# Kernel optimization log

Hardware: AMD Instinct MI355X
Metric: run time of the kernel (lower is better)

Reference implementation:

```python
import jax, jax.numpy as jnp
import numpy as np

N_SAMPLES = 8192
EMBED_DIM = 128
NUM_CLASSES = 100


def setup_inputs() -> dict:
    key = jax.random.key(0)
    k1, k2 = jax.random.split(key)
    x = jax.random.normal(k1, (N_SAMPLES, EMBED_DIM), dtype=jnp.float32)
    # FastAP assumes L2-normalized embeddings (dist2 = 2 - 2*cos in [0, 4])
    x = x / jnp.linalg.norm(x, axis=1, keepdims=True)
    labels = jax.random.randint(k2, (N_SAMPLES,), 0, NUM_CLASSES, dtype=jnp.int64 if jax.config.jax_enable_x64 else jnp.int32)
    return {"batch": x, "labels": labels, "num_bins": 10}


def reference(batch, labels, num_bins):
    N = batch.shape[0]
    L = num_bins + 1                      # number of histogram bin centers (edges of linspace)
    Delta = 4.0 / num_bins                # bin width
    Z = jnp.linspace(0.0, 4.0, L)

    same = labels[:, None] == labels[None, :]
    eye = jnp.eye(N, dtype=bool)
    I_pos = (same & ~eye).astype(batch.dtype)   # Aff > 0
    I_neg = (~same).astype(batch.dtype)         # Aff < 0 (diag is 'same', so excluded)
    N_pos = I_pos.sum(axis=1)

    # squared euclidean distance for unit-norm rows: 2 - 2*cos
    dist2 = 2.0 - 2.0 * (batch @ batch.T)       # [N, N]

    # soft-binning histogram: one N x N pulse per bin, reduced to per-row counts.
    # lax.map keeps only one [N, N] pulse buffer alive at a time.
    def bin_fn(z):
        pulse = jnp.maximum(0.0, 1.0 - jnp.abs(dist2 - z) / Delta)
        return (jnp.einsum('ij,ij->i', pulse, I_pos),
                jnp.einsum('ij,ij->i', pulse, I_neg))

    hp, hn = jax.lax.map(bin_fn, Z)             # each [L, N]
    h_pos = hp.T                                # [N, L]
    h_neg = hn.T

    H_pos = jnp.cumsum(h_pos, axis=1)
    H = jnp.cumsum(h_pos + h_neg, axis=1)

    # FastAP = h_pos * H_pos / H, with NaN/Inf (H == 0) zeroed, as in the original
    safe_H = jnp.where(H > 0, H, 1.0)
    ap = jnp.where(H > 0, h_pos * H_pos / safe_H, 0.0).sum(axis=1)

    # divide by N_pos; rows with no positives are dropped from the mean
    valid = N_pos > 0
    safe_Np = jnp.where(valid, N_pos, 1.0)
    ap = jnp.where(valid, ap / safe_Np, 0.0)

    n_valid = valid.sum().astype(batch.dtype)
    loss = 1.0 - ap.sum() / n_valid
    return loss
```

## Files before the change

### kernel.cpp

```cpp
#include <hip/hip_runtime.h>

#define NS 8192
#define EMBED 128
#define ROWCHUNK 512
#define NPANEL (ROWCHUNK / 32)
#define AROW 12
#define INV64K (1.0f / 65536.0f)

typedef __bf16 bf16x8 __attribute__((ext_vector_type(8)));
typedef float f32x4 __attribute__((ext_vector_type(4)));
typedef float f32x2 __attribute__((ext_vector_type(2)));
typedef const __attribute__((address_space(1))) unsigned ag_u32;
typedef __attribute__((address_space(3))) unsigned al_u32;

#define OFF_XB    0u
#define OFF_GS    2097152u
#define OFF_GSP   2228224u
#define OFF_GA    2359296u
#define OFF_GAP   2752512u
#define OFF_AC    3145728u
#define OFF_CNT   3145792u
#define OFF_OFS   3146304u
#define OFF_INTRA 3146816u
#define OFF_CLS   3179584u
#define ZERO_U4   65537u

__device__ inline float clamp01(float x) { return __builtin_amdgcn_fmed3f(x, 0.f, 1.f); }
__device__ inline f32x2 pkclamp01(f32x2 v) {
  return __builtin_elementwise_min(__builtin_elementwise_max(v, (f32x2){0.f, 0.f}),
                                   (f32x2){1.f, 1.f});
}
__device__ inline unsigned short f2bf(float f) {
  unsigned u = __float_as_uint(f);
  u += 0x7fffu + ((u >> 16) & 1u);
  return (unsigned short)(u >> 16);
}

__global__ __launch_bounds__(256) void prep_count_kernel(const int* __restrict__ labels,
                                                         int* __restrict__ cnt,
                                                         int* __restrict__ ofs,
                                                         int* __restrict__ intra) {
  __shared__ int c[128];
  const int tid = threadIdx.x;
  if (tid < 128) c[tid] = 0;
  __syncthreads();
  for (int i = tid; i < NS; i += 256)
    intra[i] = atomicAdd(&c[labels[i]], 1);
  __syncthreads();
  if (tid == 0) {
    int run = 0;
    for (int k = 0; k < 128; ++k) { ofs[k] = run; cnt[k] = c[k]; run += c[k]; }
  }
}

__global__ __launch_bounds__(256) void prep_scatter_kernel(
    const float* __restrict__ x, const int* __restrict__ labels,
    const int* __restrict__ ofs, const int* __restrict__ intra,
    unsigned short* __restrict__ xb, int* __restrict__ classOf,
    uint4* __restrict__ zbase) {
  const int gid = blockIdx.x * 256 + threadIdx.x;
  const int row = gid >> 4, g = gid & 15;
  const int lab = labels[row];
  const int slot = ofs[lab] + intra[row];
  const float4 v0 = reinterpret_cast<const float4*>(x)[row * 32 + g * 2];
  const float4 v1 = reinterpret_cast<const float4*>(x)[row * 32 + g * 2 + 1];
  uint4 o;
  o.x = (unsigned)f2bf(v0.x) | ((unsigned)f2bf(v0.y) << 16);
  o.y = (unsigned)f2bf(v0.z) | ((unsigned)f2bf(v0.w) << 16);
  o.z = (unsigned)f2bf(v1.x) | ((unsigned)f2bf(v1.y) << 16);
  o.w = (unsigned)f2bf(v1.z) | ((unsigned)f2bf(v1.w) << 16);
  reinterpret_cast<uint4*>(xb)[slot * 16 + (g ^ (slot & 7))] = o;
  if (g == 0) classOf[slot] = lab;
  if (gid < (int)ZERO_U4) zbase[gid] = make_uint4(0u, 0u, 0u, 0u);
}

__global__ __launch_bounds__(256, 8) void fastap_main_kernel(
    const unsigned short* __restrict__ xb,
    const int* __restrict__ classOf, const int* __restrict__ cnt,
    const int* __restrict__ ofs,
    unsigned* __restrict__ gS, unsigned* __restrict__ gSp,
    unsigned* __restrict__ gA, unsigned* __restrict__ gAp) {
  __shared__ __align__(16) unsigned short sA[2][32 * 128];

  const int tid  = threadIdx.x;
  const int wave = tid >> 6;
  const int lane = tid & 63;
  const int l16  = lane & 15;
  const int quad = lane >> 4;
  const int colBase  = blockIdx.x * 64;
  const int rowChunk = blockIdx.y * ROWCHUNK;

  const int jcol = colBase + wave * 16 + l16;
  bf16x8 bfr[4];
  #pragma unroll
  for (int kb = 0; kb < 4; ++kb) {
    const int pg = (kb * 4 + quad) ^ (l16 & 7);
    bfr[kb] = *reinterpret_cast<const bf16x8*>(&xb[jcol * 128 + pg * 8]);
  }
  const int ci = classOf[jcol];
  const int lo = ofs[ci];
  const int hi = lo + cnt[ci];

  f32x2 C01 = {0.f, 0.f}, C23 = {0.f, 0.f};
  f32x2 Cp01 = {0.f, 0.f}, Cp23 = {0.f, 0.f};

  int aOff[4];
  #pragma unroll
  for (int kb = 0; kb < 4; ++kb)
    aOff[kb] = l16 * 128 + (((kb * 4 + quad) ^ (l16 & 7)) << 3);

  const unsigned short* xrb = xb + rowChunk * 128;
  auto stage = [&](int p, int b) {
    const unsigned short* src = xrb + p * (32 * 128);
    __builtin_amdgcn_global_load_lds((ag_u32*)(src + tid * 8),
                                     (al_u32*)(&sA[b][tid * 8]), 16, 0, 0);
    __builtin_amdgcn_global_load_lds((ag_u32*)(src + (tid + 256) * 8),
                                     (al_u32*)(&sA[b][(tid + 256) * 8]), 16, 0, 0);
  };

  auto tile16 = [&](const unsigned short* ap, int lcr) {
    bf16x8 a0 = *reinterpret_cast<const bf16x8*>(&ap[aOff[0]]);
    bf16x8 a1 = *reinterpret_cast<const bf16x8*>(&ap[aOff[1]]);
    bf16x8 a2 = *reinterpret_cast<const bf16x8*>(&ap[aOff[2]]);
    bf16x8 a3 = *reinterpret_cast<const bf16x8*>(&ap[aOff[3]]);
    f32x4 acc = {0.f, 0.f, 0.f, 0.f};
    acc = __builtin_amdgcn_mfma_f32_16x16x32_bf16(a0, bfr[0], acc, 0, 0, 0);
    acc = __builtin_amdgcn_mfma_f32_16x16x32_bf16(a1, bfr[1], acc, 0, 0, 0);
    acc = __builtin_amdgcn_mfma_f32_16x16x32_bf16(a2, bfr[2], acc, 0, 0, 0);
    acc = __builtin_amdgcn_mfma_f32_16x16x32_bf16(a3, bfr[3], acc, 0, 0, 0);

    const int i0 = rowChunk + lcr + quad * 4;

    if (__builtin_expect((hi > i0) & (lo < i0 + 4), 0)) {
      #pragma unroll
      for (int r = 0; r < 4; ++r) {
        const float a = acc[r];
        const int i = i0 + r;
        const float pm = (i >= lo && i < hi) ? 1.f : 0.f;
        const f32x2 av = {a, a}, p2 = {pm, pm};
        const f32x2 d01 = pkclamp01(__builtin_elementwise_fma(av, (f32x2){5.f, 5.f},
                                                              (f32x2){-1.f, 0.f}));
        const f32x2 d23 = pkclamp01(__builtin_elementwise_fma(av, (f32x2){5.f, 5.f},
                                                              (f32x2){1.f, 2.f}));
        C01 += d01; C23 += d23;
        Cp01 = __builtin_elementwise_fma(p2, d01, Cp01);
        Cp23 = __builtin_elementwise_fma(p2, d23, Cp23);
      }
    } else {
      #pragma unroll
      for (int r = 0; r < 4; ++r) {
        const f32x2 av = {acc[r], acc[r]};
        C01 += pkclamp01(__builtin_elementwise_fma(av, (f32x2){5.f, 5.f},
                                                   (f32x2){-1.f, 0.f}));
        C23 += pkclamp01(__builtin_elementwise_fma(av, (f32x2){5.f, 5.f},
                                                   (f32x2){1.f, 2.f}));
      }
    }

    const float mabs = fmaxf(fmaxf(fabsf(acc[0]), fabsf(acc[1])),
                             fmaxf(fabsf(acc[2]), fabsf(acc[3])));
    if (__builtin_expect(mabs > 0.4f, 0)) {
      #pragma unroll
      for (int r = 0; r < 4; ++r) {
        const float a = acc[r];
        if (fabsf(a) <= 0.4f) continue;
        const int i = i0 + r;
        const float d0 = clamp01(fmaf(a, 5.f, -1.f));
        const float d1 = clamp01(a * 5.f);
        const float d2 = clamp01(fmaf(a, 5.f, 1.f));
        const float d3 = clamp01(fmaf(a, 5.f, 2.f));
        if (i == jcol) {
          C01 -= (f32x2){d0, d1};  C23 -= (f32x2){d2, d3};
          Cp01 -= (f32x2){d0, d1}; Cp23 -= (f32x2){d2, d3};
          #pragma unroll
          for (int k = 7; k <= 10; ++k)
            atomicAdd(&gA[jcol * AROW + k], (unsigned)(-65536));
        } else {
          const bool isPos = (i >= lo) & (i < hi);
          const float t = fmaf(a, -5.f, 5.f);
          #pragma unroll
          for (int k = 0; k <= 2; ++k) {
            const int q = (int)(clamp01((float)(k + 1) - t) * 65536.f + 0.5f);
            if (q) {
              atomicAdd(&gA[jcol * AROW + k], (unsigned)q);
              if (isPos) atomicAdd(&gAp[jcol * AROW + k], (unsigned)q);
            }
          }
          #pragma unroll
          for (int k = 7; k <= 10; ++k) {
            const int q = (int)((clamp01((float)(k + 1) - t) - 1.f) * 65536.f - 0.5f);
            if (q) {
              atomicAdd(&gA[jcol * AROW + k], (unsigned)q);
              if (isPos) atomicAdd(&gAp[jcol * AROW + k], (unsigned)q);
            }
          }
        }
      }
    }
  };

  stage(0, 0);
  __syncthreads();

  #pragma unroll 1
  for (int p = 0; p < NPANEL; ++p) {
    const int cur = p & 1;
    if (p + 1 < NPANEL) stage(p + 1, cur ^ 1);
    tile16(&sA[cur][0],        p * 32);
    tile16(&sA[cur][16 * 128], p * 32 + 16);
    __syncthreads();
  }

  #pragma unroll
  for (int m = 16; m < 64; m <<= 1) {
    C01.x  += __shfl_xor(C01.x,  m, 64); C01.y  += __shfl_xor(C01.y,  m, 64);
    C23.x  += __shfl_xor(C23.x,  m, 64); C23.y  += __shfl_xor(C23.y,  m, 64);
    Cp01.x += __shfl_xor(Cp01.x, m, 64); Cp01.y += __shfl_xor(Cp01.y, m, 64);
    Cp23.x += __shfl_xor(Cp23.x, m, 64); Cp23.y += __shfl_xor(Cp23.y, m, 64);
  }

  if (quad == 0) {
    const float Cv[4]  = {C01.x, C01.y, C23.x, C23.y};
    const float Cpv[4] = {Cp01.x, Cp01.y, Cp23.x, Cp23.y};
    #pragma unroll
    for (int k = 0; k < 4; ++k) {
      atomicAdd(&gS[jcol * 4 + k],  (unsigned)(int)lrintf(Cv[k]  * 65536.f));
      atomicAdd(&gSp[jcol * 4 + k], (unsigned)(int)lrintf(Cpv[k] * 65536.f));
    }
  }
}

__global__ __launch_bounds__(256) void epilogue_kernel(
    const unsigned* __restrict__ gS, const unsigned* __restrict__ gSp,
    const unsigned* __restrict__ gA, const unsigned* __restrict__ gAp,
    const int* __restrict__ classOf, const int* __restrict__ cnt,
    float* __restrict__ accum, unsigned* __restrict__ done,
    float* __restrict__ out) {
  const int i = blockIdx.x * 256 + threadIdx.x;
  const int np = cnt[classOf[i]] - 1;
  float ap = 0.f, val = 0.f, HpPrev = 0.f;
  #pragma unroll
  for (int b = 0; b <= 10; ++b) {
    const float baseH  = (b < 3) ? 0.f
                       : (b < 7) ? (float)(int)gS[i * 4 + (b - 3)]  * INV64K : 8192.f;
    const float basePp = (b < 3) ? 0.f
                       : (b < 7) ? (float)(int)gSp[i * 4 + (b - 3)] * INV64K : (float)np;
    const float H  = baseH  + (float)(int)gA[i * AROW + b]  * INV64K;
    const float Hp = basePp + (float)(int)gAp[i * AROW + b] * INV64K;
    const float hp = Hp - HpPrev;
    HpPrev = Hp;
    if (H > 1e-6f) ap += hp * Hp / H;
  }
  if (np > 0) { ap /= (float)np; val = 1.f; } else ap = 0.f;

  __shared__ float sa[256], sv[256];
  sa[threadIdx.x] = ap; sv[threadIdx.x] = val;
  __syncthreads();
  for (int s = 128; s > 0; s >>= 1) {
    if (threadIdx.x < s) {
      sa[threadIdx.x] += sa[threadIdx.x + s];
      sv[threadIdx.x] += sv[threadIdx.x + s];
    }
    __syncthreads();
  }
  if (threadIdx.x == 0) {
    atomicAdd(&accum[0], sa[0]);
    atomicAdd(&accum[1], sv[0]);
    __threadfence();
    const unsigned prev = atomicAdd(done, 1u);
    if (prev == gridDim.x - 1) {
      const float a = atomicAdd(&accum[0], 0.f);
      const float c = atomicAdd(&accum[1], 0.f);
      out[0] = 1.f - (c > 0.f ? a / c : 0.f);
    }
  }
}

extern "C" void kernel_launch(void* const* d_in, const int* in_sizes, int n_in,
                              void* d_out, int out_size, void* d_ws, size_t ws_size,
                              hipStream_t stream) {
  const float* x      = (const float*)d_in[0];
  const int*   labels = (const int*)d_in[1];
  float* out = (float*)d_out;

  char* ws = (char*)d_ws;
  unsigned short* xb = (unsigned short*)(ws + OFF_XB);
  unsigned* gS    = (unsigned*)(ws + OFF_GS);
  unsigned* gSp   = (unsigned*)(ws + OFF_GSP);
  unsigned* gA    = (unsigned*)(ws + OFF_GA);
  unsigned* gAp   = (unsigned*)(ws + OFF_GAP);
  float*    accum = (float*)(ws + OFF_AC);
  unsigned* done  = (unsigned*)(ws + OFF_AC + 8);
  int*      cnt   = (int*)(ws + OFF_CNT);
  int*      ofs   = (int*)(ws + OFF_OFS);
  int*      intra = (int*)(ws + OFF_INTRA);
  int*      cls   = (int*)(ws + OFF_CLS);

  prep_count_kernel<<<1, 256, 0, stream>>>(labels, cnt, ofs, intra);
  prep_scatter_kernel<<<512, 256, 0, stream>>>(x, labels, ofs, intra, xb, cls,
                                               (uint4*)(ws + OFF_GS));
  fastap_main_kernel<<<dim3(NS / 64, NS / ROWCHUNK), 256, 0, stream>>>(
      xb, cls, cnt, ofs, gS, gSp, gA, gAp);
  epilogue_kernel<<<NS / 256, 256, 0, stream>>>(gS, gSp, gA, gAp, cls, cnt,
                                                accum, done, out);
}
```

Before: 118.2 us.

## Compute two column tiles per wave and parallelize label counting across blocks

The main kernel now has each wave handle 32 columns (two 16-column B fragments) instead of 16. Each A fragment loaded from LDS feeds eight MFMAs instead of four, and the row chunk is halved to 256 so the grid keeps a similar block count. Launch bounds are relaxed to 6 blocks per SM to make room for the doubled accumulator registers. The single-block label count is replaced by a multi-block kernel that uses global atomics, a memset and a last-block-done prefix sum. This removes a serial launch, but adds a memset and the atomic contention that comes with it.

```diff
diff --git a/kernel.cpp b/kernel.cpp
--- a/kernel.cpp
+++ b/kernel.cpp
@@ -2,7 +2,7 @@
 
 #define NS 8192
 #define EMBED 128
-#define ROWCHUNK 512
+#define ROWCHUNK 256
 #define NPANEL (ROWCHUNK / 32)
 #define AROW 12
 #define INV64K (1.0f / 65536.0f)
@@ -21,8 +21,9 @@
 #define OFF_AC    3145728u
 #define OFF_CNT   3145792u
 #define OFF_OFS   3146304u
-#define OFF_INTRA 3146816u
-#define OFF_CLS   3179584u
+#define OFF_PD    3146816u
+#define OFF_INTRA 3146880u
+#define OFF_CLS   3179648u
 #define ZERO_U4   65537u
 
 __device__ inline float clamp01(float x) { return __builtin_amdgcn_fmed3f(x, 0.f, 1.f); }
@@ -39,17 +40,23 @@
 __global__ __launch_bounds__(256) void prep_count_kernel(const int* __restrict__ labels,
                                                          int* __restrict__ cnt,
                                                          int* __restrict__ ofs,
-                                                         int* __restrict__ intra) {
+                                                         int* __restrict__ intra,
+                                                         unsigned* __restrict__ pdone) {
+  const int gid = blockIdx.x * 256 + threadIdx.x;
+  intra[gid] = atomicAdd(&cnt[labels[gid]], 1);
+  __threadfence();
   __shared__ int c[128];
-  const int tid = threadIdx.x;
-  if (tid < 128) c[tid] = 0;
+  __shared__ unsigned last;
   __syncthreads();
-  for (int i = tid; i < NS; i += 256)
-    intra[i] = atomicAdd(&c[labels[i]], 1);
+  if (threadIdx.x == 0) last = (atomicAdd(pdone, 1u) == gridDim.x - 1) ? 1u : 0u;
   __syncthreads();
-  if (tid == 0) {
-    int run = 0;
-    for (int k = 0; k < 128; ++k) { ofs[k] = run; cnt[k] = c[k]; run += c[k]; }
+  if (last) {
+    if (threadIdx.x < 128) c[threadIdx.x] = atomicAdd(&cnt[threadIdx.x], 0);
+    __syncthreads();
+    if (threadIdx.x == 0) {
+      int run = 0;
+      for (int k = 0; k < 128; ++k) { ofs[k] = run; run += c[k]; }
+    }
   }
 }
 
@@ -74,7 +81,7 @@
   if (gid < (int)ZERO_U4) zbase[gid] = make_uint4(0u, 0u, 0u, 0u);
 }
 
-__global__ __launch_bounds__(256, 8) void fastap_main_kernel(
+__global__ __launch_bounds__(256, 6) void fastap_main_kernel(
     const unsigned short* __restrict__ xb,
     const int* __restrict__ classOf, const int* __restrict__ cnt,
     const int* __restrict__ ofs,
@@ -87,22 +94,23 @@
   const int lane = tid & 63;
   const int l16  = lane & 15;
   const int quad = lane >> 4;
-  const int colBase  = blockIdx.x * 64;
+  const int colBase  = blockIdx.x * 128;
   const int rowChunk = blockIdx.y * ROWCHUNK;
 
-  const int jcol = colBase + wave * 16 + l16;
-  bf16x8 bfr[4];
+  const int jc1 = colBase + wave * 32 + l16;
+  const int jc2 = jc1 + 16;
+  bf16x8 bf1[4], bf2[4];
   #pragma unroll
   for (int kb = 0; kb < 4; ++kb) {
     const int pg = (kb * 4 + quad) ^ (l16 & 7);
-    bfr[kb] = *reinterpret_cast<const bf16x8*>(&xb[jcol * 128 + pg * 8]);
-  }
-  const int ci = classOf[jcol];
-  const int lo = ofs[ci];
-  const int hi = lo + cnt[ci];
-
-  f32x2 C01 = {0.f, 0.f}, C23 = {0.f, 0.f};
-  f32x2 Cp01 = {0.f, 0.f}, Cp23 = {0.f, 0.f};
+    bf1[kb] = *reinterpret_cast<const bf16x8*>(&xb[jc1 * 128 + pg * 8]);
+    bf2[kb] = *reinterpret_cast<const bf16x8*>(&xb[jc2 * 128 + pg * 8]);
+  }
+  const int ci1 = classOf[jc1], lo1 = ofs[ci1], hi1 = lo1 + cnt[ci1];
+  const int ci2 = classOf[jc2], lo2 = ofs[ci2], hi2 = lo2 + cnt[ci2];
+
+  f32x2 C01a = {0.f,0.f}, C23a = {0.f,0.f}, Cp01a = {0.f,0.f}, Cp23a = {0.f,0.f};
+  f32x2 C01b = {0.f,0.f}, C23b = {0.f,0.f}, Cp01b = {0.f,0.f}, Cp23b = {0.f,0.f};
 
   int aOff[4];
   #pragma unroll
@@ -118,19 +126,8 @@
                                      (al_u32*)(&sA[b][(tid + 256) * 8]), 16, 0, 0);
   };
 
-  auto tile16 = [&](const unsigned short* ap, int lcr) {
-    bf16x8 a0 = *reinterpret_cast<const bf16x8*>(&ap[aOff[0]]);
-    bf16x8 a1 = *reinterpret_cast<const bf16x8*>(&ap[aOff[1]]);
-    bf16x8 a2 = *reinterpret_cast<const bf16x8*>(&ap[aOff[2]]);
-    bf16x8 a3 = *reinterpret_cast<const bf16x8*>(&ap[aOff[3]]);
-    f32x4 acc = {0.f, 0.f, 0.f, 0.f};
-    acc = __builtin_amdgcn_mfma_f32_16x16x32_bf16(a0, bfr[0], acc, 0, 0, 0);
-    acc = __builtin_amdgcn_mfma_f32_16x16x32_bf16(a1, bfr[1], acc, 0, 0, 0);
-    acc = __builtin_amdgcn_mfma_f32_16x16x32_bf16(a2, bfr[2], acc, 0, 0, 0);
-    acc = __builtin_amdgcn_mfma_f32_16x16x32_bf16(a3, bfr[3], acc, 0, 0, 0);
-
-    const int i0 = rowChunk + lcr + quad * 4;
-
+  auto group = [&](const f32x4& acc, int jc, int lo, int hi, int i0,
+                   f32x2& C01, f32x2& C23, f32x2& Cp01, f32x2& Cp23) {
     if (__builtin_expect((hi > i0) & (lo < i0 + 4), 0)) {
       #pragma unroll
       for (int r = 0; r < 4; ++r) {
@@ -169,12 +166,12 @@
         const float d1 = clamp01(a * 5.f);
         const float d2 = clamp01(fmaf(a, 5.f, 1.f));
         const float d3 = clamp01(fmaf(a, 5.f, 2.f));
-        if (i == jcol) {
+        if (i == jc) {
           C01 -= (f32x2){d0, d1};  C23 -= (f32x2){d2, d3};
           Cp01 -= (f32x2){d0, d1}; Cp23 -= (f32x2){d2, d3};
           #pragma unroll
           for (int k = 7; k <= 10; ++k)
-            atomicAdd(&gA[jcol * AROW + k], (unsigned)(-65536));
+            atomicAdd(&gA[jc * AROW + k], (unsigned)(-65536));
         } else {
           const bool isPos = (i >= lo) & (i < hi);
           const float t = fmaf(a, -5.f, 5.f);
@@ -182,21 +179,41 @@
           for (int k = 0; k <= 2; ++k) {
             const int q = (int)(clamp01((float)(k + 1) - t) * 65536.f + 0.5f);
             if (q) {
-              atomicAdd(&gA[jcol * AROW + k], (unsigned)q);
-              if (isPos) atomicAdd(&gAp[jcol * AROW + k], (unsigned)q);
+              atomicAdd(&gA[jc * AROW + k], (unsigned)q);
+              if (isPos) atomicAdd(&gAp[jc * AROW + k], (unsigned)q);
             }
           }
           #pragma unroll
           for (int k = 7; k <= 10; ++k) {
             const int q = (int)((clamp01((float)(k + 1) - t) - 1.f) * 65536.f - 0.5f);
             if (q) {
-              atomicAdd(&gA[jcol * AROW + k], (unsigned)q);
-              if (isPos) atomicAdd(&gAp[jcol * AROW + k], (unsigned)q);
+              atomicAdd(&gA[jc * AROW + k], (unsigned)q);
+              if (isPos) atomicAdd(&gAp[jc * AROW + k], (unsigned)q);
             }
           }
         }
       }
     }
+  };
+
+  auto tile16 = [&](const unsigned short* ap, int lcr) {
+    bf16x8 a0 = *reinterpret_cast<const bf16x8*>(&ap[aOff[0]]);
+    bf16x8 a1 = *reinterpret_cast<const bf16x8*>(&ap[aOff[1]]);
+    bf16x8 a2 = *reinterpret_cast<const bf16x8*>(&ap[aOff[2]]);
+    bf16x8 a3 = *reinterpret_cast<const bf16x8*>(&ap[aOff[3]]);
+    f32x4 acc1 = {0.f, 0.f, 0.f, 0.f}, acc2 = {0.f, 0.f, 0.f, 0.f};
+    acc1 = __builtin_amdgcn_mfma_f32_16x16x32_bf16(a0, bf1[0], acc1, 0, 0, 0);
+    acc1 = __builtin_amdgcn_mfma_f32_16x16x32_bf16(a1, bf1[1], acc1, 0, 0, 0);
+    acc1 = __builtin_amdgcn_mfma_f32_16x16x32_bf16(a2, bf1[2], acc1, 0, 0, 0);
+    acc1 = __builtin_amdgcn_mfma_f32_16x16x32_bf16(a3, bf1[3], acc1, 0, 0, 0);
+    acc2 = __builtin_amdgcn_mfma_f32_16x16x32_bf16(a0, bf2[0], acc2, 0, 0, 0);
+    acc2 = __builtin_amdgcn_mfma_f32_16x16x32_bf16(a1, bf2[1], acc2, 0, 0, 0);
+    acc2 = __builtin_amdgcn_mfma_f32_16x16x32_bf16(a2, bf2[2], acc2, 0, 0, 0);
+    acc2 = __builtin_amdgcn_mfma_f32_16x16x32_bf16(a3, bf2[3], acc2, 0, 0, 0);
+
+    const int i0 = rowChunk + lcr + quad * 4;
+    group(acc1, jc1, lo1, hi1, i0, C01a, C23a, Cp01a, Cp23a);
+    group(acc2, jc2, lo2, hi2, i0, C01b, C23b, Cp01b, Cp23b);
   };
 
   stage(0, 0);
@@ -213,19 +230,27 @@
 
   #pragma unroll
   for (int m = 16; m < 64; m <<= 1) {
-    C01.x  += __shfl_xor(C01.x,  m, 64); C01.y  += __shfl_xor(C01.y,  m, 64);
-    C23.x  += __shfl_xor(C23.x,  m, 64); C23.y  += __shfl_xor(C23.y,  m, 64);
-    Cp01.x += __shfl_xor(Cp01.x, m, 64); Cp01.y += __shfl_xor(Cp01.y, m, 64);
-    Cp23.x += __shfl_xor(Cp23.x, m, 64); Cp23.y += __shfl_xor(Cp23.y, m, 64);
+    C01a.x += __shfl_xor(C01a.x, m, 64); C01a.y += __shfl_xor(C01a.y, m, 64);
+    C23a.x += __shfl_xor(C23a.x, m, 64); C23a.y += __shfl_xor(C23a.y, m, 64);
+    Cp01a.x += __shfl_xor(Cp01a.x, m, 64); Cp01a.y += __shfl_xor(Cp01a.y, m, 64);
+    Cp23a.x += __shfl_xor(Cp23a.x, m, 64); Cp23a.y += __shfl_xor(Cp23a.y, m, 64);
+    C01b.x += __shfl_xor(C01b.x, m, 64); C01b.y += __shfl_xor(C01b.y, m, 64);
+    C23b.x += __shfl_xor(C23b.x, m, 64); C23b.y += __shfl_xor(C23b.y, m, 64);
+    Cp01b.x += __shfl_xor(Cp01b.x, m, 64); Cp01b.y += __shfl_xor(Cp01b.y, m, 64);
+    Cp23b.x += __shfl_xor(Cp23b.x, m, 64); Cp23b.y += __shfl_xor(Cp23b.y, m, 64);
   }
 
   if (quad == 0) {
-    const float Cv[4]  = {C01.x, C01.y, C23.x, C23.y};
-    const float Cpv[4] = {Cp01.x, Cp01.y, Cp23.x, Cp23.y};
+    const float Cv1[4]  = {C01a.x, C01a.y, C23a.x, C23a.y};
+    const float Cpv1[4] = {Cp01a.x, Cp01a.y, Cp23a.x, Cp23a.y};
+    const float Cv2[4]  = {C01b.x, C01b.y, C23b.x, C23b.y};
+    const float Cpv2[4] = {Cp01b.x, Cp01b.y, Cp23b.x, Cp23b.y};
     #pragma unroll
     for (int k = 0; k < 4; ++k) {
-      atomicAdd(&gS[jcol * 4 + k],  (unsigned)(int)lrintf(Cv[k]  * 65536.f));
-      atomicAdd(&gSp[jcol * 4 + k], (unsigned)(int)lrintf(Cpv[k] * 65536.f));
+      atomicAdd(&gS[jc1 * 4 + k],  (unsigned)(int)lrintf(Cv1[k]  * 65536.f));
+      atomicAdd(&gSp[jc1 * 4 + k], (unsigned)(int)lrintf(Cpv1[k] * 65536.f));
+      atomicAdd(&gS[jc2 * 4 + k],  (unsigned)(int)lrintf(Cv2[k]  * 65536.f));
+      atomicAdd(&gSp[jc2 * 4 + k], (unsigned)(int)lrintf(Cpv2[k] * 65536.f));
     }
   }
 }
@@ -293,13 +318,15 @@
   unsigned* done  = (unsigned*)(ws + OFF_AC + 8);
   int*      cnt   = (int*)(ws + OFF_CNT);
   int*      ofs   = (int*)(ws + OFF_OFS);
+  unsigned* pdone = (unsigned*)(ws + OFF_PD);
   int*      intra = (int*)(ws + OFF_INTRA);
   int*      cls   = (int*)(ws + OFF_CLS);
 
-  prep_count_kernel<<<1, 256, 0, stream>>>(labels, cnt, ofs, intra);
+  hipMemsetAsync(ws + OFF_CNT, 0, 1088, stream);
+  prep_count_kernel<<<NS / 256, 256, 0, stream>>>(labels, cnt, ofs, intra, pdone);
   prep_scatter_kernel<<<512, 256, 0, stream>>>(x, labels, ofs, intra, xb, cls,
                                                (uint4*)(ws + OFF_GS));
-  fastap_main_kernel<<<dim3(NS / 64, NS / ROWCHUNK), 256, 0, stream>>>(
+  fastap_main_kernel<<<dim3(NS / 128, NS / ROWCHUNK), 256, 0, stream>>>(
       xb, cls, cnt, ofs, gS, gSp, gA, gAp);
   epilogue_kernel<<<NS / 256, 256, 0, stream>>>(gS, gSp, gA, gAp, cls, cnt,
                                                 accum, done, out);
```

Result: slower. 448.9 us (+279.9%).
